# Kernel tuning notes

Hardware: AMD Instinct MI355X
Metric: run time of the kernel (lower is better)

## Reference

```python
import jax, jax.numpy as jnp
import numpy as np

NNODES = 128
BS = 1024
MAX_ST = (NNODES + 1) ** 2   # 16641
MAX_ST1 = NNODES ** 2        # 16384
AT_LEN = NNODES + 1          # 129
MAXOUT = AT_LEN + MAX_ST + MAX_ST1  # 33154
HIDDEN = 512
OUT_DIM = AT_LEN             # 129


def setup_inputs() -> dict:
    key = jax.random.key(0)
    ks = jax.random.split(key, 6)
    st = jax.random.normal(ks[0], (BS, MAX_ST), dtype=jnp.float32)
    at = jax.random.normal(ks[1], (BS, AT_LEN), dtype=jnp.float32)
    st1 = jax.random.normal(ks[2], (BS, MAX_ST1), dtype=jnp.float32)
    # MLP params (self.layers): Linear(MAXOUT->HIDDEN) + ReLU + Linear(HIDDEN->OUT_DIM)
    W1 = jax.random.normal(ks[3], (MAXOUT, HIDDEN), dtype=jnp.float32) * (1.0 / np.sqrt(MAXOUT))
    b1 = jnp.zeros((HIDDEN,), dtype=jnp.float32)
    W2 = jax.random.normal(ks[4], (HIDDEN, OUT_DIM), dtype=jnp.float32) * (1.0 / np.sqrt(HIDDEN))
    b2 = jnp.zeros((OUT_DIM,), dtype=jnp.float32)
    return {"st": st, "at": at, "st1": st1, "W1": W1, "b1": b1, "W2": W2, "b2": b2}


def reference(st, at, st1, W1, b1, W2, b2):
    # Batched equivalent of the per-sample Python loop:
    # per sample: cat(pad(st.flatten(), maxSt), at, pad(st1.flatten(), maxSt1)) -> layers -> cat outputs.
    # st/st1 are already at padded sizes here, so concat directly along features.
    x = jnp.concatenate([st, at, st1], axis=1)          # [B, MAXOUT]
    h = jax.nn.relu(x @ W1 + b1)                        # [B, HIDDEN]
    out = h @ W2 + b2                                   # [B, OUT_DIM]
    return out.reshape(-1)                              # concatenated 1-D outputs, matching torch.cat
```

## Files before the change

### kernel.cpp

```cpp
#include <hip/hip_runtime.h>

#define BATCH 1024
#define STSZ 16641
#define ATSZ 129
#define ST1SZ 16384
#define K1 33154
#define K1P 33280
#define HID 512
#define ODIM 129
#define NKT 520
#define NSLICE 32

typedef __bf16 bf16;
typedef bf16 bf16x8 __attribute__((ext_vector_type(8)));
typedef float floatx4 __attribute__((ext_vector_type(4)));
typedef float f32x4u __attribute__((ext_vector_type(4), aligned(4)));

typedef __attribute__((address_space(3))) unsigned int as3_uint;
typedef __attribute__((address_space(1))) unsigned int as1_uint;

__device__ __forceinline__ unsigned short f2bf(float f) {
  unsigned int u = __float_as_uint(f);
  unsigned int r = (u + 0x7FFFu + ((u >> 16) & 1u)) >> 16;
  return (unsigned short)r;
}
__device__ __forceinline__ float bf2f(unsigned short s) {
  unsigned int u = ((unsigned int)s) << 16;
  return __uint_as_float(u);
}

__device__ __forceinline__ void gload_lds16(const unsigned short* g, unsigned short* l) {
  __builtin_amdgcn_global_load_lds((const as1_uint*)g, (as3_uint*)l, 16, 0, 0);
}

__global__ __launch_bounds__(256) void packX(const float* __restrict__ st,
                                             const float* __restrict__ at,
                                             const float* __restrict__ st1,
                                             unsigned short* __restrict__ Xb) {
  int b = blockIdx.y;
  int g = blockIdx.x * 256 + threadIdx.x;
  if (g >= K1P / 4) return;
  int col = g * 4;
  const float* srow  = st  + (long)b * STSZ;
  const float* arow  = at  + (long)b * ATSZ;
  const float* s1row = st1 + (long)b * ST1SZ;

  float4 v;
  if (col + 3 < STSZ) {
    f32x4u t = *(const f32x4u*)(srow + col);
    v = make_float4(t.x, t.y, t.z, t.w);
  } else if (col >= STSZ + ATSZ && col + 3 < K1) {
    f32x4u t = *(const f32x4u*)(s1row + (col - (STSZ + ATSZ)));
    v = make_float4(t.x, t.y, t.z, t.w);
  } else if (col >= STSZ && col + 3 < STSZ + ATSZ) {
    f32x4u t = *(const f32x4u*)(arow + (col - STSZ));
    v = make_float4(t.x, t.y, t.z, t.w);
  } else if (col >= K1) {
    v = make_float4(0.f, 0.f, 0.f, 0.f);
  } else {
    float e[4];
#pragma unroll
    for (int j = 0; j < 4; ++j) {
      int p = col + j;
      if (p < STSZ)                 e[j] = srow[p];
      else if (p < STSZ + ATSZ)     e[j] = arow[p - STSZ];
      else if (p < K1)              e[j] = s1row[p - (STSZ + ATSZ)];
      else                          e[j] = 0.f;
    }
    v = make_float4(e[0], e[1], e[2], e[3]);
  }
  unsigned short o[4] = { f2bf(v.x), f2bf(v.y), f2bf(v.z), f2bf(v.w) };
  *(ushort4*)&Xb[(long)b * K1P + col] = *(const ushort4*)o;
}

__global__ __launch_bounds__(256) void packW1(const float* __restrict__ W1,
                                              unsigned short* __restrict__ W1t) {
  __shared__ unsigned short tile[64][72];
  int k0 = blockIdx.x * 64;
  int n0 = blockIdx.y * 64;
  int tid = threadIdx.x;
  int nt = (tid & 15) * 4;
  int kr = tid >> 4;
#pragma unroll
  for (int p = 0; p < 4; ++p) {
    int k = p * 16 + kr;
    int kk = k0 + k;
    float4 v = make_float4(0.f, 0.f, 0.f, 0.f);
    if (kk < K1) v = *(const float4*)&W1[(long)kk * HID + n0 + nt];
    unsigned short o[4] = { f2bf(v.x), f2bf(v.y), f2bf(v.z), f2bf(v.w) };
    *(ushort4*)&tile[k][nt] = *(const ushort4*)o;
  }
  __syncthreads();
  int kt = (tid & 15) * 4;
  int nr = tid >> 4;
#pragma unroll
  for (int p = 0; p < 4; ++p) {
    int n = p * 16 + nr;
    unsigned short o[4] = { tile[kt][n], tile[kt + 1][n], tile[kt + 2][n], tile[kt + 3][n] };
    *(ushort4*)&W1t[(long)(n0 + n) * K1P + k0 + kt] = *(const ushort4*)o;
  }
}

__global__ __launch_bounds__(256, 2) void gemm1(const unsigned short* __restrict__ Xb,
                                                const unsigned short* __restrict__ W1t,
                                                unsigned short* __restrict__ part) {
  __shared__ __align__(16) unsigned short lA[128 * 64];
  __shared__ __align__(16) unsigned short lB[128 * 64];

  int nt = blockIdx.x;
  int mt = blockIdx.y;
  int s  = blockIdx.z;
  int t0 = s * 16 + (s < 8 ? s : 8);
  int tc = 16 + (s < 8 ? 1 : 0);

  int tid = threadIdx.x;
  int wave = tid >> 6;
  int lane = tid & 63;
  int wm = (wave & 1) * 64;
  int wn = (wave >> 1) * 64;

  floatx4 acc[4][4] = {};

  const unsigned short* Ab = Xb  + (long)(mt * 128) * K1P;
  const unsigned short* Bb = W1t + (long)(nt * 128) * K1P;

  int srow = lane >> 3;
  int scol = ((lane & 7) ^ srow) * 8;

  int sr = lane & 7;

  for (int it = 0; it < tc; ++it) {
    long kOff = (long)(t0 + it) * 64;
#pragma unroll
    for (int r = 0; r < 4; ++r) {
      int c = wave * 4 + r;
      int row = c * 8 + srow;
      gload_lds16(Ab + (long)row * K1P + kOff + scol, &lA[c * 512 + lane * 8]);
      gload_lds16(Bb + (long)row * K1P + kOff + scol, &lB[c * 512 + lane * 8]);
    }
    __syncthreads();
#pragma unroll
    for (int ks = 0; ks < 2; ++ks) {
      int q = ks * 4 + (lane >> 4);
      int kidx = ((q ^ sr)) * 8;
      bf16x8 af[4], bfr[4];
#pragma unroll
      for (int i = 0; i < 4; ++i)
        af[i] = *(const bf16x8*)&lA[(wm + i * 16 + (lane & 15)) * 64 + kidx];
#pragma unroll
      for (int j = 0; j < 4; ++j)
        bfr[j] = *(const bf16x8*)&lB[(wn + j * 16 + (lane & 15)) * 64 + kidx];
#pragma unroll
      for (int i = 0; i < 4; ++i)
#pragma unroll
        for (int j = 0; j < 4; ++j)
          acc[i][j] = __builtin_amdgcn_mfma_f32_16x16x32_bf16(af[i], bfr[j], acc[i][j], 0, 0, 0);
    }
    __syncthreads();
  }

  unsigned short* P = part + (long)s * BATCH * HID;
  int cn = nt * 128 + wn + (lane & 15);
  int rbase = mt * 128 + wm + (lane >> 4) * 4;
#pragma unroll
  for (int i = 0; i < 4; ++i)
#pragma unroll
    for (int j = 0; j < 4; ++j)
#pragma unroll
      for (int r = 0; r < 4; ++r)
        P[(long)(rbase + i * 16 + r) * HID + cn + j * 16] = f2bf(acc[i][j][r]);
}

__global__ __launch_bounds__(256) void reduceBias(const unsigned short* __restrict__ part,
                                                  const float* __restrict__ b1,
                                                  float* __restrict__ h) {
  int e4 = blockIdx.x * 256 + threadIdx.x;
  float4 a = ((const float4*)b1)[e4 & (HID / 4 - 1)];
#pragma unroll
  for (int s = 0; s < NSLICE; ++s) {
    ushort4 p = ((const ushort4*)part)[(long)s * (BATCH * HID / 4) + e4];
    a.x += bf2f(p.x); a.y += bf2f(p.y); a.z += bf2f(p.z); a.w += bf2f(p.w);
  }
  a.x = fmaxf(a.x, 0.f); a.y = fmaxf(a.y, 0.f);
  a.z = fmaxf(a.z, 0.f); a.w = fmaxf(a.w, 0.f);
  ((float4*)h)[e4] = a;
}

__global__ __launch_bounds__(256) void gemm2(const float* __restrict__ h,
                                             const float* __restrict__ W2,
                                             const float* __restrict__ b2,
                                             float* __restrict__ out) {
  __shared__ float hs[HID];
  int m = blockIdx.x;
  int t = threadIdx.x;
#pragma unroll
  for (int i = t; i < HID; i += 256) hs[i] = h[(long)m * HID + i];
  __syncthreads();
  if (t < ODIM) {
    float a = b2[t];
#pragma unroll 8
    for (int k = 0; k < HID; ++k) a += hs[k] * W2[k * ODIM + t];
    out[(long)m * ODIM + t] = a;
  }
}

extern "C" void kernel_launch(void* const* d_in, const int* in_sizes, int n_in,
                              void* d_out, int out_size, void* d_ws, size_t ws_size,
                              hipStream_t stream) {
  const float* st  = (const float*)d_in[0];
  const float* at  = (const float*)d_in[1];
  const float* st1 = (const float*)d_in[2];
  const float* W1  = (const float*)d_in[3];
  const float* b1  = (const float*)d_in[4];
  const float* W2  = (const float*)d_in[5];
  const float* b2  = (const float*)d_in[6];
  float* out = (float*)d_out;

  char* ws = (char*)d_ws;
  unsigned short* Xb   = (unsigned short*)ws;
  unsigned short* W1t  = (unsigned short*)(ws + (size_t)BATCH * K1P * 2);
  unsigned short* part = (unsigned short*)(ws + (size_t)BATCH * K1P * 2 + (size_t)HID * K1P * 2);
  float* h = (float*)(ws + (size_t)BATCH * K1P * 2 + (size_t)HID * K1P * 2
                      + (size_t)NSLICE * BATCH * HID * 2);

  packX<<<dim3((K1P / 4 + 255) / 256, BATCH), 256, 0, stream>>>(st, at, st1, Xb);
  packW1<<<dim3(NKT, HID / 64), 256, 0, stream>>>(W1, W1t);
  gemm1<<<dim3(4, 8, NSLICE), 256, 0, stream>>>(Xb, W1t, part);
  reduceBias<<<dim3(BATCH * HID / 4 / 256), 256, 0, stream>>>(part, b1, h);
  gemm2<<<dim3(BATCH), 256, 0, stream>>>(h, W2, b2, out);
}
```

Before: 323.6 us.

## Fuse X fp32-to-bf16 packing into gemm1 A-tile loads

Removes the separate packX kernel and has gemm1 read st/at/st1 directly in fp32, convert to bf16 in registers, and store the swizzled A tile into LDS. This avoids writing and re-reading a bf16 copy of X (about 68 MB of write plus read) but makes each of the 4 N-tile blocks re-read fp32 X, doubling the bytes per A load. It also bumps launch_bounds occupancy hint from 2 to 3 blocks per CU, and A loads now go through registers synchronously instead of async global_load_lds.

```diff
diff --git a/kernel.cpp b/kernel.cpp
--- a/kernel.cpp
+++ b/kernel.cpp
@@ -15,6 +15,7 @@
 typedef bf16 bf16x8 __attribute__((ext_vector_type(8)));
 typedef float floatx4 __attribute__((ext_vector_type(4)));
 typedef float f32x4u __attribute__((ext_vector_type(4), aligned(4)));
+typedef unsigned short ushort8v __attribute__((ext_vector_type(8)));
 
 typedef __attribute__((address_space(3))) unsigned int as3_uint;
 typedef __attribute__((address_space(1))) unsigned int as1_uint;
@@ -33,44 +34,41 @@
   __builtin_amdgcn_global_load_lds((const as1_uint*)g, (as3_uint*)l, 16, 0, 0);
 }
 
-__global__ __launch_bounds__(256) void packX(const float* __restrict__ st,
-                                             const float* __restrict__ at,
-                                             const float* __restrict__ st1,
-                                             unsigned short* __restrict__ Xb) {
-  int b = blockIdx.y;
-  int g = blockIdx.x * 256 + threadIdx.x;
-  if (g >= K1P / 4) return;
-  int col = g * 4;
-  const float* srow  = st  + (long)b * STSZ;
-  const float* arow  = at  + (long)b * ATSZ;
-  const float* s1row = st1 + (long)b * ST1SZ;
-
-  float4 v;
-  if (col + 3 < STSZ) {
-    f32x4u t = *(const f32x4u*)(srow + col);
-    v = make_float4(t.x, t.y, t.z, t.w);
-  } else if (col >= STSZ + ATSZ && col + 3 < K1) {
-    f32x4u t = *(const f32x4u*)(s1row + (col - (STSZ + ATSZ)));
-    v = make_float4(t.x, t.y, t.z, t.w);
-  } else if (col >= STSZ && col + 3 < STSZ + ATSZ) {
-    f32x4u t = *(const f32x4u*)(arow + (col - STSZ));
-    v = make_float4(t.x, t.y, t.z, t.w);
+__device__ __forceinline__ void loadA8(const float* __restrict__ st,
+                                       const float* __restrict__ at,
+                                       const float* __restrict__ st1,
+                                       int row, int col, float f[8]) {
+  if (col + 7 < STSZ) {
+    const float* p = st + (long)row * STSZ + col;
+    f32x4u a = *(const f32x4u*)p;
+    f32x4u b = *(const f32x4u*)(p + 4);
+    f[0] = a.x; f[1] = a.y; f[2] = a.z; f[3] = a.w;
+    f[4] = b.x; f[5] = b.y; f[6] = b.z; f[7] = b.w;
+  } else if (col >= STSZ + ATSZ && col + 7 < K1) {
+    const float* p = st1 + (long)row * ST1SZ + (col - (STSZ + ATSZ));
+    f32x4u a = *(const f32x4u*)p;
+    f32x4u b = *(const f32x4u*)(p + 4);
+    f[0] = a.x; f[1] = a.y; f[2] = a.z; f[3] = a.w;
+    f[4] = b.x; f[5] = b.y; f[6] = b.z; f[7] = b.w;
+  } else if (col >= STSZ && col + 7 < STSZ + ATSZ) {
+    const float* p = at + (long)row * ATSZ + (col - STSZ);
+    f32x4u a = *(const f32x4u*)p;
+    f32x4u b = *(const f32x4u*)(p + 4);
+    f[0] = a.x; f[1] = a.y; f[2] = a.z; f[3] = a.w;
+    f[4] = b.x; f[5] = b.y; f[6] = b.z; f[7] = b.w;
   } else if (col >= K1) {
-    v = make_float4(0.f, 0.f, 0.f, 0.f);
+#pragma unroll
+    for (int j = 0; j < 8; ++j) f[j] = 0.f;
   } else {
-    float e[4];
-#pragma unroll
-    for (int j = 0; j < 4; ++j) {
+#pragma unroll
+    for (int j = 0; j < 8; ++j) {
       int p = col + j;
-      if (p < STSZ)                 e[j] = srow[p];
-      else if (p < STSZ + ATSZ)     e[j] = arow[p - STSZ];
-      else if (p < K1)              e[j] = s1row[p - (STSZ + ATSZ)];
-      else                          e[j] = 0.f;
-    }
-    v = make_float4(e[0], e[1], e[2], e[3]);
-  }
-  unsigned short o[4] = { f2bf(v.x), f2bf(v.y), f2bf(v.z), f2bf(v.w) };
-  *(ushort4*)&Xb[(long)b * K1P + col] = *(const ushort4*)o;
+      if (p < STSZ)               f[j] = st[(long)row * STSZ + p];
+      else if (p < STSZ + ATSZ)   f[j] = at[(long)row * ATSZ + (p - STSZ)];
+      else if (p < K1)            f[j] = st1[(long)row * ST1SZ + (p - (STSZ + ATSZ))];
+      else                        f[j] = 0.f;
+    }
+  }
 }
 
 __global__ __launch_bounds__(256) void packW1(const float* __restrict__ W1,
@@ -101,7 +99,9 @@
   }
 }
 
-__global__ __launch_bounds__(256, 2) void gemm1(const unsigned short* __restrict__ Xb,
+__global__ __launch_bounds__(256, 3) void gemm1(const float* __restrict__ st,
+                                                const float* __restrict__ at,
+                                                const float* __restrict__ st1,
                                                 const unsigned short* __restrict__ W1t,
                                                 unsigned short* __restrict__ part) {
   __shared__ __align__(16) unsigned short lA[128 * 64];
@@ -121,7 +121,6 @@
 
   floatx4 acc[4][4] = {};
 
-  const unsigned short* Ab = Xb  + (long)(mt * 128) * K1P;
   const unsigned short* Bb = W1t + (long)(nt * 128) * K1P;
 
   int srow = lane >> 3;
@@ -130,13 +129,23 @@
   int sr = lane & 7;
 
   for (int it = 0; it < tc; ++it) {
-    long kOff = (long)(t0 + it) * 64;
+    int kOff = (t0 + it) * 64;
 #pragma unroll
     for (int r = 0; r < 4; ++r) {
       int c = wave * 4 + r;
       int row = c * 8 + srow;
-      gload_lds16(Ab + (long)row * K1P + kOff + scol, &lA[c * 512 + lane * 8]);
       gload_lds16(Bb + (long)row * K1P + kOff + scol, &lB[c * 512 + lane * 8]);
+    }
+#pragma unroll
+    for (int r = 0; r < 4; ++r) {
+      int c = wave * 4 + r;
+      int row = mt * 128 + c * 8 + srow;
+      float f[8];
+      loadA8(st, at, st1, row, kOff + scol, f);
+      ushort8v o;
+#pragma unroll
+      for (int j = 0; j < 8; ++j) o[j] = f2bf(f[j]);
+      *(ushort8v*)&lA[c * 512 + lane * 8] = o;
     }
     __syncthreads();
 #pragma unroll
@@ -217,15 +226,12 @@
   float* out = (float*)d_out;
 
   char* ws = (char*)d_ws;
-  unsigned short* Xb   = (unsigned short*)ws;
-  unsigned short* W1t  = (unsigned short*)(ws + (size_t)BATCH * K1P * 2);
-  unsigned short* part = (unsigned short*)(ws + (size_t)BATCH * K1P * 2 + (size_t)HID * K1P * 2);
-  float* h = (float*)(ws + (size_t)BATCH * K1P * 2 + (size_t)HID * K1P * 2
-                      + (size_t)NSLICE * BATCH * HID * 2);
-
-  packX<<<dim3((K1P / 4 + 255) / 256, BATCH), 256, 0, stream>>>(st, at, st1, Xb);
+  unsigned short* W1t  = (unsigned short*)ws;
+  unsigned short* part = (unsigned short*)(ws + (size_t)HID * K1P * 2);
+  float* h = (float*)(ws + (size_t)HID * K1P * 2 + (size_t)NSLICE * BATCH * HID * 2);
+
   packW1<<<dim3(NKT, HID / 64), 256, 0, stream>>>(W1, W1t);
-  gemm1<<<dim3(4, 8, NSLICE), 256, 0, stream>>>(Xb, W1t, part);
+  gemm1<<<dim3(4, 8, NSLICE), 256, 0, stream>>>(st, at, st1, W1t, part);
   reduceBias<<<dim3(BATCH * HID / 4 / 256), 256, 0, stream>>>(part, b1, h);
   gemm2<<<dim3(BATCH), 256, 0, stream>>>(h, W2, b2, out);
 }
```

After: 363.1 us. 12.2% more time.

## Merge pack kernels, fuse reduce with gemm2, remap gemm1 blocks per XCD

Applied to the files above, without the earlier changes.

Combines packX and packW1 into one launch and folds the split-K reduction, bias and ReLU into the second GEMM, so the h buffer and two launches go away. gemm1 now uses a flattened 1D grid that groups the K-slices and M tiles sharing data onto the same XCD, to improve L2 reuse. Its launch bounds rise to 4 blocks per CU. gemm2 uses four partial accumulators for more ILP. The risks are register pressure from the occupancy hint and divergent LDS use inside the merged pack kernel.

```diff
diff --git a/kernel.cpp b/kernel.cpp
--- a/kernel.cpp
+++ b/kernel.cpp
@@ -10,6 +10,8 @@
 #define ODIM 129
 #define NKT 520
 #define NSLICE 32
+#define NPACKX (33 * 1024)
+#define NPACKW (NKT * 8)
 
 typedef __bf16 bf16;
 typedef bf16 bf16x8 __attribute__((ext_vector_type(8)));
@@ -33,83 +35,92 @@
   __builtin_amdgcn_global_load_lds((const as1_uint*)g, (as3_uint*)l, 16, 0, 0);
 }
 
-__global__ __launch_bounds__(256) void packX(const float* __restrict__ st,
-                                             const float* __restrict__ at,
-                                             const float* __restrict__ st1,
-                                             unsigned short* __restrict__ Xb) {
-  int b = blockIdx.y;
-  int g = blockIdx.x * 256 + threadIdx.x;
-  if (g >= K1P / 4) return;
-  int col = g * 4;
-  const float* srow  = st  + (long)b * STSZ;
-  const float* arow  = at  + (long)b * ATSZ;
-  const float* s1row = st1 + (long)b * ST1SZ;
-
-  float4 v;
-  if (col + 3 < STSZ) {
-    f32x4u t = *(const f32x4u*)(srow + col);
-    v = make_float4(t.x, t.y, t.z, t.w);
-  } else if (col >= STSZ + ATSZ && col + 3 < K1) {
-    f32x4u t = *(const f32x4u*)(s1row + (col - (STSZ + ATSZ)));
-    v = make_float4(t.x, t.y, t.z, t.w);
-  } else if (col >= STSZ && col + 3 < STSZ + ATSZ) {
-    f32x4u t = *(const f32x4u*)(arow + (col - STSZ));
-    v = make_float4(t.x, t.y, t.z, t.w);
-  } else if (col >= K1) {
-    v = make_float4(0.f, 0.f, 0.f, 0.f);
+__global__ __launch_bounds__(256) void packAll(const float* __restrict__ st,
+                                               const float* __restrict__ at,
+                                               const float* __restrict__ st1,
+                                               const float* __restrict__ W1,
+                                               unsigned short* __restrict__ Xb,
+                                               unsigned short* __restrict__ W1t) {
+  __shared__ unsigned short tile[64][72];
+  int bb  = blockIdx.x;
+  int tid = threadIdx.x;
+
+  if (bb < NPACKX) {
+    int bx = bb % 33;
+    int b  = bb / 33;
+    int g  = bx * 256 + tid;
+    if (g >= K1P / 4) return;
+    int col = g * 4;
+    const float* srow  = st  + (long)b * STSZ;
+    const float* arow  = at  + (long)b * ATSZ;
+    const float* s1row = st1 + (long)b * ST1SZ;
+
+    float4 v;
+    if (col + 3 < STSZ) {
+      f32x4u t = *(const f32x4u*)(srow + col);
+      v = make_float4(t.x, t.y, t.z, t.w);
+    } else if (col >= STSZ + ATSZ && col + 3 < K1) {
+      f32x4u t = *(const f32x4u*)(s1row + (col - (STSZ + ATSZ)));
+      v = make_float4(t.x, t.y, t.z, t.w);
+    } else if (col >= STSZ && col + 3 < STSZ + ATSZ) {
+      f32x4u t = *(const f32x4u*)(arow + (col - STSZ));
+      v = make_float4(t.x, t.y, t.z, t.w);
+    } else if (col >= K1) {
+      v = make_float4(0.f, 0.f, 0.f, 0.f);
+    } else {
+      float e[4];
+#pragma unroll
+      for (int j = 0; j < 4; ++j) {
+        int p = col + j;
+        if (p < STSZ)                 e[j] = srow[p];
+        else if (p < STSZ + ATSZ)     e[j] = arow[p - STSZ];
+        else if (p < K1)              e[j] = s1row[p - (STSZ + ATSZ)];
+        else                          e[j] = 0.f;
+      }
+      v = make_float4(e[0], e[1], e[2], e[3]);
+    }
+    unsigned short o[4] = { f2bf(v.x), f2bf(v.y), f2bf(v.z), f2bf(v.w) };
+    *(ushort4*)&Xb[(long)b * K1P + col] = *(const ushort4*)o;
   } else {
-    float e[4];
-#pragma unroll
-    for (int j = 0; j < 4; ++j) {
-      int p = col + j;
-      if (p < STSZ)                 e[j] = srow[p];
-      else if (p < STSZ + ATSZ)     e[j] = arow[p - STSZ];
-      else if (p < K1)              e[j] = s1row[p - (STSZ + ATSZ)];
-      else                          e[j] = 0.f;
-    }
-    v = make_float4(e[0], e[1], e[2], e[3]);
-  }
-  unsigned short o[4] = { f2bf(v.x), f2bf(v.y), f2bf(v.z), f2bf(v.w) };
-  *(ushort4*)&Xb[(long)b * K1P + col] = *(const ushort4*)o;
-}
-
-__global__ __launch_bounds__(256) void packW1(const float* __restrict__ W1,
-                                              unsigned short* __restrict__ W1t) {
-  __shared__ unsigned short tile[64][72];
-  int k0 = blockIdx.x * 64;
-  int n0 = blockIdx.y * 64;
-  int tid = threadIdx.x;
-  int nt = (tid & 15) * 4;
-  int kr = tid >> 4;
-#pragma unroll
-  for (int p = 0; p < 4; ++p) {
-    int k = p * 16 + kr;
-    int kk = k0 + k;
-    float4 v = make_float4(0.f, 0.f, 0.f, 0.f);
-    if (kk < K1) v = *(const float4*)&W1[(long)kk * HID + n0 + nt];
-    unsigned short o[4] = { f2bf(v.x), f2bf(v.y), f2bf(v.z), f2bf(v.w) };
-    *(ushort4*)&tile[k][nt] = *(const ushort4*)o;
-  }
-  __syncthreads();
-  int kt = (tid & 15) * 4;
-  int nr = tid >> 4;
-#pragma unroll
-  for (int p = 0; p < 4; ++p) {
-    int n = p * 16 + nr;
-    unsigned short o[4] = { tile[kt][n], tile[kt + 1][n], tile[kt + 2][n], tile[kt + 3][n] };
-    *(ushort4*)&W1t[(long)(n0 + n) * K1P + k0 + kt] = *(const ushort4*)o;
-  }
-}
-
-__global__ __launch_bounds__(256, 2) void gemm1(const unsigned short* __restrict__ Xb,
+    int lb = bb - NPACKX;
+    int k0 = (lb % NKT) * 64;
+    int n0 = (lb / NKT) * 64;
+    int nt = (tid & 15) * 4;
+    int kr = tid >> 4;
+#pragma unroll
+    for (int p = 0; p < 4; ++p) {
+      int k = p * 16 + kr;
+      int kk = k0 + k;
+      float4 v = make_float4(0.f, 0.f, 0.f, 0.f);
+      if (kk < K1) v = *(const float4*)&W1[(long)kk * HID + n0 + nt];
+      unsigned short o[4] = { f2bf(v.x), f2bf(v.y), f2bf(v.z), f2bf(v.w) };
+      *(ushort4*)&tile[k][nt] = *(const ushort4*)o;
+    }
+    __syncthreads();
+    int kt = (tid & 15) * 4;
+    int nr = tid >> 4;
+#pragma unroll
+    for (int p = 0; p < 4; ++p) {
+      int n = p * 16 + nr;
+      unsigned short o[4] = { tile[kt][n], tile[kt + 1][n], tile[kt + 2][n], tile[kt + 3][n] };
+      *(ushort4*)&W1t[(long)(n0 + n) * K1P + k0 + kt] = *(const ushort4*)o;
+    }
+  }
+}
+
+__global__ __launch_bounds__(256, 4) void gemm1(const unsigned short* __restrict__ Xb,
                                                 const unsigned short* __restrict__ W1t,
                                                 unsigned short* __restrict__ part) {
   __shared__ __align__(16) unsigned short lA[128 * 64];
   __shared__ __align__(16) unsigned short lB[128 * 64];
 
-  int nt = blockIdx.x;
-  int mt = blockIdx.y;
-  int s  = blockIdx.z;
+  int hB  = blockIdx.x;
+  int xcd = hB & 7;
+  int idx = hB >> 3;
+  int gidx = xcd * 32 + (idx >> 2);
+  int nt = idx & 3;
+  int mt = gidx & 7;
+  int s  = gidx >> 3;
   int t0 = s * 16 + (s < 8 ? s : 8);
   int tc = 16 + (s < 8 ? 1 : 0);
 
@@ -171,36 +182,37 @@
         P[(long)(rbase + i * 16 + r) * HID + cn + j * 16] = f2bf(acc[i][j][r]);
 }
 
-__global__ __launch_bounds__(256) void reduceBias(const unsigned short* __restrict__ part,
-                                                  const float* __restrict__ b1,
-                                                  float* __restrict__ h) {
-  int e4 = blockIdx.x * 256 + threadIdx.x;
-  float4 a = ((const float4*)b1)[e4 & (HID / 4 - 1)];
-#pragma unroll
-  for (int s = 0; s < NSLICE; ++s) {
-    ushort4 p = ((const ushort4*)part)[(long)s * (BATCH * HID / 4) + e4];
-    a.x += bf2f(p.x); a.y += bf2f(p.y); a.z += bf2f(p.z); a.w += bf2f(p.w);
-  }
-  a.x = fmaxf(a.x, 0.f); a.y = fmaxf(a.y, 0.f);
-  a.z = fmaxf(a.z, 0.f); a.w = fmaxf(a.w, 0.f);
-  ((float4*)h)[e4] = a;
-}
-
-__global__ __launch_bounds__(256) void gemm2(const float* __restrict__ h,
-                                             const float* __restrict__ W2,
-                                             const float* __restrict__ b2,
-                                             float* __restrict__ out) {
+__global__ __launch_bounds__(256) void reduceGemm2(const unsigned short* __restrict__ part,
+                                                   const float* __restrict__ b1,
+                                                   const float* __restrict__ W2,
+                                                   const float* __restrict__ b2,
+                                                   float* __restrict__ out) {
   __shared__ float hs[HID];
   int m = blockIdx.x;
   int t = threadIdx.x;
-#pragma unroll
-  for (int i = t; i < HID; i += 256) hs[i] = h[(long)m * HID + i];
+
+  float2 bv = ((const float2*)b1)[t];
+  float a0 = bv.x, a1 = bv.y;
+#pragma unroll
+  for (int s = 0; s < NSLICE; ++s) {
+    unsigned int u = *(const unsigned int*)&part[((long)s * BATCH + m) * HID + 2 * t];
+    a0 += bf2f((unsigned short)(u & 0xffffu));
+    a1 += bf2f((unsigned short)(u >> 16));
+  }
+  hs[2 * t]     = fmaxf(a0, 0.f);
+  hs[2 * t + 1] = fmaxf(a1, 0.f);
   __syncthreads();
+
   if (t < ODIM) {
-    float a = b2[t];
-#pragma unroll 8
-    for (int k = 0; k < HID; ++k) a += hs[k] * W2[k * ODIM + t];
-    out[(long)m * ODIM + t] = a;
+    float c0 = 0.f, c1 = 0.f, c2 = 0.f, c3 = 0.f;
+#pragma unroll 4
+    for (int k = 0; k < HID; k += 4) {
+      c0 += hs[k]     * W2[(long)(k)     * ODIM + t];
+      c1 += hs[k + 1] * W2[(long)(k + 1) * ODIM + t];
+      c2 += hs[k + 2] * W2[(long)(k + 2) * ODIM + t];
+      c3 += hs[k + 3] * W2[(long)(k + 3) * ODIM + t];
+    }
+    out[(long)m * ODIM + t] = ((c0 + c1) + (c2 + c3)) + b2[t];
   }
 }
 
@@ -220,12 +232,8 @@
   unsigned short* Xb   = (unsigned short*)ws;
   unsigned short* W1t  = (unsigned short*)(ws + (size_t)BATCH * K1P * 2);
   unsigned short* part = (unsigned short*)(ws + (size_t)BATCH * K1P * 2 + (size_t)HID * K1P * 2);
-  float* h = (float*)(ws + (size_t)BATCH * K1P * 2 + (size_t)HID * K1P * 2
-                      + (size_t)NSLICE * BATCH * HID * 2);
-
-  packX<<<dim3((K1P / 4 + 255) / 256, BATCH), 256, 0, stream>>>(st, at, st1, Xb);
-  packW1<<<dim3(NKT, HID / 64), 256, 0, stream>>>(W1, W1t);
-  gemm1<<<dim3(4, 8, NSLICE), 256, 0, stream>>>(Xb, W1t, part);
-  reduceBias<<<dim3(BATCH * HID / 4 / 256), 256, 0, stream>>>(part, b1, h);
-  gemm2<<<dim3(BATCH), 256, 0, stream>>>(h, W2, b2, out);
-}
+
+  packAll<<<dim3(NPACKX + NPACKW), 256, 0, stream>>>(st, at, st1, W1, Xb, W1t);
+  gemm1<<<dim3(1024), 256, 0, stream>>>(Xb, W1t, part);
+  reduceGemm2<<<dim3(BATCH), 256, 0, stream>>>(part, b1, W2, b2, out);
+}
```

Result: faster. 299.4 us (-7.5%).
